# Optimization experiments

Measured on AMD Instinct MI355X. Metric: run time of the kernel, lower is better.

## Reference

```python
import jax, jax.numpy as jnp
import numpy as np

EPS = 1e-5

def setup_inputs() -> dict:
    key = jax.random.key(0)
    ks = jax.random.split(key, 12)
    b, C, Hx = 8, 1024, 28          # x: (b, C, Hx, Hx); y: (b, C//2, 2*Hx, 2*Hx)
    C2 = C // 2
    r = C2 // 7                      # fc bottleneck = 73
    f32 = jnp.float32
    inp = {
        'y': jax.random.normal(ks[0], (b, C2, 2*Hx, 2*Hx), f32),
        'x': jax.random.normal(ks[1], (b, C, Hx, Hx), f32),
        'fc1_w': jax.random.normal(ks[2], (r, C2), f32) * 0.02,
        'fc2_w': jax.random.normal(ks[3], (C2, r), f32) * 0.02,
        'conv_w': jax.random.normal(ks[4], (C2, C, 1, 1), f32) * 0.02,
        'conv_b': jnp.zeros((C2,), f32),
        'conv1_w': jax.random.normal(ks[5], (C2, C2 * 4, 1, 1), f32) * 0.02,
        'conv1_b': jnp.zeros((C2,), f32),
        'bn_gamma': jnp.ones((C2,), f32),
        'bn_beta': jnp.zeros((C2,), f32),
        'bn_mean': jnp.zeros((C2,), f32),
        'bn_var': jnp.ones((C2,), f32),
        'dw_w': jax.random.normal(ks[6], (C, 1, 3, 3), f32) * 0.1,  # depthwise, groups=C
        'dw_b': jnp.zeros((C,), f32),
    }
    return inp

def reference(y, x, fc1_w, fc2_w, conv_w, conv_b, conv1_w, conv1_b,
              bn_gamma, bn_beta, bn_mean, bn_var, dw_w, dw_b):
    def bn(t):  # BatchNorm2d in eval mode (running stats); same bn module reused twice
        return (t - bn_mean[:, None, None]) * jax.lax.rsqrt(bn_var[:, None, None] + EPS) \
               * bn_gamma[:, None, None] + bn_beta[:, None, None]
    # SE channel attention on y
    s = jnp.mean(y, axis=(2, 3))                              # (b, C2) GAP
    s = jax.nn.relu(s @ fc1_w.T) @ fc2_w.T                    # bias-free FCs
    y1 = y * jax.nn.sigmoid(s)[:, :, None, None]
    # depthwise 3x3 conv on x
    x1 = jax.lax.conv_general_dilated(
        x, dw_w, (1, 1), ((1, 1), (1, 1)),
        feature_group_count=x.shape[1],
        dimension_numbers=('NCHW', 'OIHW', 'NCHW')) + dw_b[None, :, None, None]
    # np.cov per (b, c) map: rows are variables, ddof=1 -> (Xc @ Xc^T)/(W-1)
    Wn = x1.shape[-1]
    xc = x1 - jnp.mean(x1, axis=-1, keepdims=True)
    x2 = jnp.einsum('bchw,bcgw->bchg', xc, xc) / (Wn - 1)     # (b, C, H, H)
    # 1x1 conv C->C2, bn, sigmoid
    x2 = jnp.einsum('bchw,oc->bohw', x2, conv_w[:, :, 0, 0]) + conv_b[None, :, None, None]
    x2 = jax.nn.sigmoid(bn(x2))
    # bilinear upsample x2 (half-pixel == torch align_corners=False)
    def up2(t):
        bb, cc, hh, ww = t.shape
        return jax.image.resize(t, (bb, cc, 2 * hh, 2 * ww), method='bilinear')
    x_up = up2(x)
    x2_up = up2(x2)
    cat = jnp.concatenate([y1, x2_up, x_up], axis=1)          # (b, 4*C2, 2H, 2W)
    out = jnp.einsum('bchw,oc->bohw', cat, conv1_w[:, :, 0, 0]) + conv1_b[None, :, None, None]
    return jax.nn.relu(bn(out))
```

## Files before the change

kernel.cpp:

```cpp
#include <hip/hip_runtime.h>
#include <math.h>

#define EPSV 1e-5f
#define B 8
#define C 1024
#define C2 512
#define RK 73
#define HW 784
#define QW 3136

typedef __attribute__((ext_vector_type(8))) short bf16x8;
typedef __attribute__((ext_vector_type(4))) float f32x4;

__device__ __forceinline__ unsigned short f2bf(float f) {
    unsigned u = __float_as_uint(f);
    return (unsigned short)((u + 0x7fffu + ((u >> 16) & 1u)) >> 16);
}
__device__ __forceinline__ float ld_f(const float* p) { return *p; }
__device__ __forceinline__ float ld_f(const unsigned short* p) {
    return __uint_as_float(((unsigned)*p) << 16);
}
__device__ __forceinline__ void ld4f(const float* p, float* d) {
    float4 v = *(const float4*)p;
    d[0] = v.x; d[1] = v.y; d[2] = v.z; d[3] = v.w;
}
__device__ __forceinline__ void ld4f(const unsigned short* p, float* d) {
    uint2 u = *(const uint2*)p;
    d[0] = __uint_as_float((u.x & 0xffffu) << 16);
    d[1] = __uint_as_float(u.x & 0xffff0000u);
    d[2] = __uint_as_float((u.y & 0xffffu) << 16);
    d[3] = __uint_as_float(u.y & 0xffff0000u);
}

__global__ void zero_s0(float* __restrict__ s0) {
    s0[blockIdx.x * 256 + threadIdx.x] = 0.f;
}

__global__ void se_fc_kernel(const float* __restrict__ s0,
                             const float* __restrict__ fc1_w,
                             const float* __restrict__ fc2_w,
                             float* __restrict__ att) {
    int b = blockIdx.x;
    __shared__ float sv[C2];
    __shared__ float hv[RK];
    for (int i = threadIdx.x; i < C2; i += 256) sv[i] = s0[b * C2 + i] * (1.0f / QW);
    __syncthreads();
    if (threadIdx.x < RK) {
        float acc = 0.f;
        const float4* wr4 = (const float4*)(fc1_w + threadIdx.x * C2);
        const float4* sv4 = (const float4*)sv;
#pragma unroll 16
        for (int k = 0; k < C2 / 4; ++k) {
            float4 w4 = wr4[k], s4 = sv4[k];
            acc += w4.x * s4.x + w4.y * s4.y + w4.z * s4.z + w4.w * s4.w;
        }
        hv[threadIdx.x] = fmaxf(acc, 0.f);
    }
    __syncthreads();
    for (int o = threadIdx.x; o < C2; o += 256) {
        float acc = 0.f;
        const float* wr = fc2_w + o * RK;
#pragma unroll
        for (int j = 0; j < RK; ++j) acc += wr[j] * hv[j];
        att[b * C2 + o] = 1.f / (1.f + expf(-acc));
    }
}

__global__ void dwcov_kernel(const float* __restrict__ x,
                             const float* __restrict__ dw_w,
                             const float* __restrict__ dw_b,
                             unsigned short* __restrict__ cov) {
    int bc = blockIdx.x;
    int c = bc & (C - 1);
    __shared__ float xs[HW];
    __shared__ __align__(16) float x1[HW];
    __shared__ float rm[28];
    const float* px = x + (size_t)bc * HW;
    for (int i = threadIdx.x; i < HW; i += 256) xs[i] = px[i];
    float wk[9];
#pragma unroll
    for (int j = 0; j < 9; ++j) wk[j] = dw_w[c * 9 + j];
    float bias = dw_b[c];
    __syncthreads();
    for (int p = threadIdx.x; p < HW; p += 256) {
        int h = p / 28, w = p - h * 28;
        float acc = bias;
#pragma unroll
        for (int dh = 0; dh < 3; ++dh) {
            int hh = h + dh - 1;
            if (hh < 0 || hh >= 28) continue;
#pragma unroll
            for (int dw = 0; dw < 3; ++dw) {
                int ww = w + dw - 1;
                if (ww < 0 || ww >= 28) continue;
                acc += xs[hh * 28 + ww] * wk[dh * 3 + dw];
            }
        }
        x1[p] = acc;
    }
    __syncthreads();
    if (threadIdx.x < 28) {
        float s = 0.f;
        for (int w = 0; w < 28; ++w) s += x1[threadIdx.x * 28 + w];
        rm[threadIdx.x] = s * (1.f / 28.f);
    }
    __syncthreads();
    unsigned short* pc = cov + (size_t)bc * HW;
    for (int idx = threadIdx.x; idx < 406; idx += 256) {
        int h = (int)((sqrtf((float)(8 * idx + 1)) - 1.f) * 0.5f);
        while ((h + 1) * (h + 2) / 2 <= idx) ++h;
        while (h * (h + 1) / 2 > idx) --h;
        int g = idx - h * (h + 1) / 2;
        float mh = rm[h], mg = rm[g];
        const float4* xh = (const float4*)&x1[h * 28];
        const float4* xg = (const float4*)&x1[g * 28];
        float acc = 0.f;
#pragma unroll
        for (int w4 = 0; w4 < 7; ++w4) {
            float4 a = xh[w4], bq = xg[w4];
            acc += (a.x - mh) * (bq.x - mg);
            acc += (a.y - mh) * (bq.y - mg);
            acc += (a.z - mh) * (bq.z - mg);
            acc += (a.w - mh) * (bq.w - mg);
        }
        unsigned short v = f2bf(acc * (1.f / 27.f));
        pc[h * 28 + g] = v;
        pc[g * 28 + h] = v;
    }
}

__global__ void pack_w(const float* __restrict__ conv_w, const float* __restrict__ conv_b,
                       const float* __restrict__ conv1_w, const float* __restrict__ conv1_b,
                       const float* __restrict__ bn_g, const float* __restrict__ bn_b,
                       const float* __restrict__ bn_m, const float* __restrict__ bn_v,
                       const float* __restrict__ att,
                       unsigned short* __restrict__ w0b, unsigned short* __restrict__ w1y,
                       unsigned short* __restrict__ w1pT,
                       float* __restrict__ sA, float* __restrict__ sB0, float* __restrict__ sB1) {
    int o = blockIdx.x, t = threadIdx.x;
    {
        int c4 = t * 4;
        float4 w4 = *(const float4*)&conv_w[(size_t)o * C + c4];
        unsigned short pk[4] = { f2bf(w4.x), f2bf(w4.y), f2bf(w4.z), f2bf(w4.w) };
        *(uint2*)&w0b[(size_t)o * C + c4] = *(uint2*)pk;
    }
#pragma unroll
    for (int i = 0; i < 2; ++i) {
        int e = t + i * 256;
        if (e < 384) {
            int c4 = e * 4;
            float4 w4 = *(const float4*)&conv1_w[(size_t)o * 2048 + 512 + c4];
            unsigned short pk[4] = { f2bf(w4.x), f2bf(w4.y), f2bf(w4.z), f2bf(w4.w) };
            *(uint2*)&w1pT[(size_t)o * 1536 + c4] = *(uint2*)pk;
        }
    }
#pragma unroll
    for (int i = 0; i < 4; ++i) {
        int e = t + i * 256;
        int bb = e >> 7, c4 = (e & 127) * 4;
        float4 w4 = *(const float4*)&conv1_w[(size_t)o * 2048 + c4];
        float4 a4 = *(const float4*)&att[bb * C2 + c4];
        unsigned short pk[4] = { f2bf(w4.x * a4.x), f2bf(w4.y * a4.y),
                                 f2bf(w4.z * a4.z), f2bf(w4.w * a4.w) };
        *(uint2*)&w1y[((size_t)bb * C2 + o) * C2 + c4] = *(uint2*)pk;
    }
    if (t == 0) {
        float sc = rsqrtf(bn_v[o] + EPSV) * bn_g[o];
        float bi = bn_b[o] - bn_m[o] * sc;
        sA[o] = sc;
        sB0[o] = conv_b[o] * sc + bi;
        sB1[o] = conv1_b[o] * sc + bi;
    }
}

template<typename ST, bool GAP>
__global__ __launch_bounds__(256)
void transpose_pass(const ST* __restrict__ src, unsigned short* __restrict__ dst,
                    float* __restrict__ s0,
                    int rows, int cols, int dpitch, int doff) {
    int b = blockIdx.z;
    int c0 = blockIdx.y * 64, p0 = blockIdx.x * 64;
    __shared__ float ts[64][65];
    int tid = threadIdx.x;
    int pl4 = (tid & 15) * 4, rr = tid >> 4;
    const ST* sb = src + ((size_t)b * rows + c0) * cols + p0;
    if (p0 + pl4 < cols) {
#pragma unroll
        for (int j = 0; j < 4; ++j) {
            int cl = rr + j * 16;
            float d[4];
            ld4f(&sb[(size_t)cl * cols + pl4], d);
            ts[cl][pl4 + 0] = d[0]; ts[cl][pl4 + 1] = d[1];
            ts[cl][pl4 + 2] = d[2]; ts[cl][pl4 + 3] = d[3];
        }
    }
    __syncthreads();
    int pl2b = tid >> 3, cl0 = (tid & 7) * 8;
#pragma unroll
    for (int j = 0; j < 2; ++j) {
        int pl2 = pl2b + j * 32;
        if (p0 + pl2 < cols) {
            unsigned short pk[8];
#pragma unroll
            for (int i = 0; i < 8; ++i) pk[i] = f2bf(ts[cl0 + i][pl2]);
            *(uint4*)&dst[((size_t)b * cols + p0 + pl2) * dpitch + doff + c0 + cl0] = *(uint4*)pk;
        }
    }
    if (GAP) {
        if (tid < 64) {
            float s = 0.f;
#pragma unroll
            for (int i = 0; i < 64; ++i) s += ts[tid][i];
            atomicAdd(&s0[b * rows + c0 + tid], s);
        }
    }
}

template<int MODE, int K>
__global__ __launch_bounds__(256)
void mfma_gemm(const unsigned short* __restrict__ wpk,
               const unsigned short* __restrict__ bsrc,
               const unsigned short* __restrict__ Pb,
               const float* __restrict__ sA, const float* __restrict__ sB,
               void* __restrict__ outv) {
    constexpr int NIT = K / 64;
    constexpr int NT  = (MODE == 2) ? 49 : 98;
    constexpr int QN = NT >> 3, REM = NT & 7;
    int bx = blockIdx.x;
    int r = bx & 7, ii = bx >> 3;
    int og = ii & 7, s = ii >> 3;
    int cnt = QN + (r < REM ? 1 : 0);
    if (s >= cnt) return;
    int t = (r < REM ? r * (QN + 1) : REM * (QN + 1) + (r - REM) * QN) + s;
    int o0 = og * 64;
    int n0 = t * 64;
    int b = blockIdx.z;
    union SM {
        struct { __align__(16) unsigned short Wt[2][4096]; __align__(16) unsigned short At[2][4096]; } s;
        float pt[(MODE == 2) ? 64 * 84 : 4];
    };
    __shared__ SM sm;
    int tid = threadIdx.x;
    int lane = tid & 63, wv = tid >> 6;
    int ln = lane & 15, quad = lane >> 4;
    int o_w = (wv >> 1) * 32, q_w = (wv & 1) * 32;
    int r_ = tid >> 2, cq = tid & 3;
    int stw0 = r_ * 64 + ((( cq << 1)      ^ (r_ & 7)) << 3);
    int stw1 = r_ * 64 + ((((cq << 1) | 1) ^ (r_ & 7)) << 3);
    int rq0 = (( quad      ^ (ln & 7)) << 3);
    int rq1 = (((4 | quad) ^ (ln & 7)) << 3);
    const unsigned short* wp = (MODE == 2) ? wpk + (size_t)b * C2 * C2 : wpk;
    const unsigned short* wg = wp + (size_t)(o0 + r_) * K + cq * 16;
    const unsigned short* bg = bsrc + ((size_t)((MODE == 2) ? b * QW : 0) + n0 + r_) * K + cq * 16;

    uint4 stA_a0, stA_a1, stA_b0, stA_b1;
    uint4 stB_a0, stB_a1, stB_b0, stB_b1;
    uint4 stC_a0, stC_a1, stC_b0, stC_b1;
    uint4 stD_a0, stD_a1, stD_b0, stD_b1;

#define LD_STAGE(P, CH) {                                                   \
        P##_a0 = *(const uint4*)(wg + (size_t)(CH) * 64);                   \
        P##_a1 = *(const uint4*)(wg + (size_t)(CH) * 64 + 8);               \
        P##_b0 = *(const uint4*)(bg + (size_t)(CH) * 64);                   \
        P##_b1 = *(const uint4*)(bg + (size_t)(CH) * 64 + 8); }

#define ST_STAGE(P, BUF) {                                                  \
        *(uint4*)&sm.s.Wt[BUF][stw0] = P##_a0;                              \
        *(uint4*)&sm.s.Wt[BUF][stw1] = P##_a1;                              \
        *(uint4*)&sm.s.At[BUF][stw0] = P##_b0;                              \
        *(uint4*)&sm.s.At[BUF][stw1] = P##_b1; }

#define GEMM_BODY(BUF, P, CHW, CHL) {                                               \
        bf16x8 a0 = *(const bf16x8*)&sm.s.Wt[BUF][(o_w + ln) * 64 + rq0];           \
        bf16x8 a1 = *(const bf16x8*)&sm.s.Wt[BUF][(o_w + 16 + ln) * 64 + rq0];      \
        bf16x8 b0 = *(const bf16x8*)&sm.s.At[BUF][(q_w + ln) * 64 + rq0];           \
        bf16x8 b1 = *(const bf16x8*)&sm.s.At[BUF][(q_w + 16 + ln) * 64 + rq0];      \
        bf16x8 a2 = *(const bf16x8*)&sm.s.Wt[BUF][(o_w + ln) * 64 + rq1];           \
        bf16x8 a3 = *(const bf16x8*)&sm.s.Wt[BUF][(o_w + 16 + ln) * 64 + rq1];      \
        bf16x8 b2 = *(const bf16x8*)&sm.s.At[BUF][(q_w + ln) * 64 + rq1];           \
        bf16x8 b3 = *(const bf16x8*)&sm.s.At[BUF][(q_w + 16 + ln) * 64 + rq1];      \
        acc[0][0] = __builtin_amdgcn_mfma_f32_16x16x32_bf16(a0, b0, acc[0][0], 0, 0, 0); \
        acc[0][1] = __builtin_amdgcn_mfma_f32_16x16x32_bf16(a0, b1, acc[0][1], 0, 0, 0); \
        acc[1][0] = __builtin_amdgcn_mfma_f32_16x16x32_bf16(a1, b0, acc[1][0], 0, 0, 0); \
        acc[1][1] = __builtin_amdgcn_mfma_f32_16x16x32_bf16(a1, b1, acc[1][1], 0, 0, 0); \
        acc[0][0] = __builtin_amdgcn_mfma_f32_16x16x32_bf16(a2, b2, acc[0][0], 0, 0, 0); \
        acc[0][1] = __builtin_amdgcn_mfma_f32_16x16x32_bf16(a2, b3, acc[0][1], 0, 0, 0); \
        acc[1][0] = __builtin_amdgcn_mfma_f32_16x16x32_bf16(a3, b2, acc[1][0], 0, 0, 0); \
        acc[1][1] = __builtin_amdgcn_mfma_f32_16x16x32_bf16(a3, b3, acc[1][1], 0, 0, 0); \
        if ((CHW) < NIT) {                                                          \
            ST_STAGE(P, (BUF) ^ 1)                                                  \
            if ((CHL) < NIT) LD_STAGE(P, (CHL))                                     \
            asm volatile("s_waitcnt lgkmcnt(0)" ::: "memory");                      \
            __builtin_amdgcn_s_barrier();                                           \
            __builtin_amdgcn_sched_barrier(0);                                      \
        } }

    LD_STAGE(stA, 0)
    ST_STAGE(stA, 0)
    LD_STAGE(stB, 1)
    LD_STAGE(stC, 2)
    LD_STAGE(stD, 3)
    LD_STAGE(stA, 4)
    asm volatile("s_waitcnt lgkmcnt(0)" ::: "memory");
    __builtin_amdgcn_s_barrier();
    __builtin_amdgcn_sched_barrier(0);

    f32x4 acc[2][2] = {};
    for (int i2 = 0; i2 < NIT; i2 += 4) {
        GEMM_BODY(0, stB, i2 + 1, i2 + 5)
        GEMM_BODY(1, stC, i2 + 2, i2 + 6)
        GEMM_BODY(0, stD, i2 + 3, i2 + 7)
        GEMM_BODY(1, stA, i2 + 4, i2 + 8)
    }
#undef GEMM_BODY
#undef ST_STAGE
#undef LD_STAGE

    if (MODE == 2) {
        float* outp = (float*)outv;
        int h0 = n0 / 56;
        int hmin = (h0 & 1) ? (h0 >> 1) : max(0, (h0 >> 1) - 1);
        float stv[21];
#pragma unroll
        for (int j = 0; j < 21; ++j) {
            int e = tid + j * 256;
            int o_l = e / 84, rem = e - o_l * 84;
            int s2 = rem / 28, w = rem - s2 * 28;
            int row = min(hmin + s2, 27);
            stv[j] = ld_f(&Pb[((size_t)b * C2 + o0 + o_l) * HW + row * 28 + w]);
        }
        __syncthreads();
#pragma unroll
        for (int j = 0; j < 21; ++j) sm.pt[tid + j * 256] = stv[j];
        __syncthreads();
#pragma unroll
        for (int nt = 0; nt < 2; ++nt) {
            int q = n0 + q_w + nt * 16 + ln;
            int hq = q / 56, wq = q - hq * 56;
            int hm = hq >> 1, wm = wq >> 1;
            int hn = (hq & 1) ? min(hm + 1, 27) : max(hm - 1, 0);
            int wn_ = (wq & 1) ? min(wm + 1, 27) : max(wm - 1, 0);
            int rm_ = (hm - hmin) * 28, rn_ = (hn - hmin) * 28;
#pragma unroll
            for (int mt = 0; mt < 2; ++mt)
#pragma unroll
                for (int reg = 0; reg < 4; ++reg) {
                    int ol = o_w + mt * 16 + quad * 4 + reg;
                    int o = o0 + ol;
                    const float* Pt = &sm.pt[ol * 84];
                    float up = 0.5625f * Pt[rm_ + wm] + 0.1875f * (Pt[rm_ + wn_] + Pt[rn_ + wm])
                             + 0.0625f * Pt[rn_ + wn_];
                    float v = (acc[mt][nt][reg] + up) * sA[o] + sB[o];
                    outp[((size_t)b * C2 + o) * QW + q] = fmaxf(v, 0.f);
                }
        }
    } else if (MODE == 0) {
        unsigned short* outp = (unsigned short*)outv;
#pragma unroll
        for (int nt = 0; nt < 2; ++nt) {
            int n = n0 + q_w + nt * 16 + ln;
#pragma unroll
            for (int mt = 0; mt < 2; ++mt) {
                int ob = o0 + o_w + mt * 16 + quad * 4;
                unsigned short pk[4];
#pragma unroll
                for (int reg = 0; reg < 4; ++reg) {
                    int o = ob + reg;
                    float v = acc[mt][nt][reg] * sA[o] + sB[o];
                    pk[reg] = f2bf(1.f / (1.f + expf(-v)));
                }
                *(uint2*)&outp[(size_t)n * 1536 + ob] = *(uint2*)pk;
            }
        }
    } else {
        unsigned short* outp = (unsigned short*)outv;
#pragma unroll
        for (int nt = 0; nt < 2; ++nt) {
            int n = n0 + q_w + nt * 16 + ln;
            int be = n / HW, pe = n - be * HW;
#pragma unroll
            for (int mt = 0; mt < 2; ++mt)
#pragma unroll
                for (int reg = 0; reg < 4; ++reg) {
                    int o = o0 + o_w + mt * 16 + quad * 4 + reg;
                    outp[((size_t)be * C2 + o) * HW + pe] = f2bf(acc[mt][nt][reg]);
                }
        }
    }
}

extern "C" void kernel_launch(void* const* d_in, const int* in_sizes, int n_in,
                              void* d_out, int out_size, void* d_ws, size_t ws_size,
                              hipStream_t stream) {
    const float* y       = (const float*)d_in[0];
    const float* x       = (const float*)d_in[1];
    const float* fc1_w   = (const float*)d_in[2];
    const float* fc2_w   = (const float*)d_in[3];
    const float* conv_w  = (const float*)d_in[4];
    const float* conv_b  = (const float*)d_in[5];
    const float* conv1_w = (const float*)d_in[6];
    const float* conv1_b = (const float*)d_in[7];
    const float* bn_g    = (const float*)d_in[8];
    const float* bn_b    = (const float*)d_in[9];
    const float* bn_m    = (const float*)d_in[10];
    const float* bn_v    = (const float*)d_in[11];
    const float* dw_w    = (const float*)d_in[12];
    const float* dw_b    = (const float*)d_in[13];
    float* out = (float*)d_out;

    unsigned short* cov_bf = (unsigned short*)d_out;
    unsigned short* covT   = cov_bf + (size_t)B * C * HW;
    unsigned short* BcatT  = covT + (size_t)B * HW * C;

    float* ws  = (float*)d_ws;
    float* s0  = ws;
    float* att = ws + 4096;
    float* sA  = ws + 8192;
    float* sB0 = ws + 8704;
    float* sB1 = ws + 9216;
    unsigned short* w0b  = (unsigned short*)(ws + 9728);
    unsigned short* w1y  = w0b + (size_t)C2 * C;
    unsigned short* w1pT = w1y + (size_t)B * C2 * C2;
    unsigned short* yT   = w1pT + (size_t)C2 * 1536;
    unsigned short* Pb   = yT + (size_t)B * QW * C2;

    zero_s0<<<16, 256, 0, stream>>>(s0);
    transpose_pass<float, true><<<dim3(49, 8, B), 256, 0, stream>>>(
        y, yT, s0, C2, QW, C2, 0);
    se_fc_kernel<<<B, 256, 0, stream>>>(s0, fc1_w, fc2_w, att);
    pack_w<<<C2, 256, 0, stream>>>(conv_w, conv_b, conv1_w, conv1_b,
                                   bn_g, bn_b, bn_m, bn_v, att,
                                   w0b, w1y, w1pT, sA, sB0, sB1);
    dwcov_kernel<<<B * C, 256, 0, stream>>>(x, dw_w, dw_b, cov_bf);
    transpose_pass<float, false><<<dim3(13, 16, B), 256, 0, stream>>>(
        x, BcatT, nullptr, C, HW, 1536, 512);
    transpose_pass<unsigned short, false><<<dim3(13, 16, B), 256, 0, stream>>>(
        cov_bf, covT, nullptr, C, HW, C, 0);
    mfma_gemm<0, 1024><<<dim3(832), 256, 0, stream>>>(w0b, covT, nullptr, sA, sB0, BcatT);
    mfma_gemm<1, 1536><<<dim3(832), 256, 0, stream>>>(w1pT, BcatT, nullptr, sA, sB0, Pb);
    mfma_gemm<2, 512><<<dim3(448, 1, B), 256, 0, stream>>>(w1y, yT, Pb, sA, sB1, out);
}
```

Before: 284.8 us.

## Fuse cov transpose into MODE-0 GEMM loads and process two channels per dwcov block

Removes the separate bf16 transpose of the covariance tensor. The MODE-0 GEMM now reads channel-major cov directly, using strided 32-bit loads that it repacks into the swizzled shared-memory layout, and tiles per batch over 13 pixel tiles. The depthwise/cov kernel handles two channels per block with float4 loads, which halves the block count. This saves a full read-write pass over the cov tensor and one launch, at the cost of less coalesced GEMM operand loads and some padded work on the last pixel tile.

Result: faster. 274.1 us (-3.8%).

```diff
diff --git a/kernel.cpp b/kernel.cpp
--- a/kernel.cpp
+++ b/kernel.cpp
@@ -71,61 +71,78 @@
                              const float* __restrict__ dw_b,
                              unsigned short* __restrict__ cov) {
     int bc = blockIdx.x;
-    int c = bc & (C - 1);
-    __shared__ float xs[HW];
-    __shared__ __align__(16) float x1[HW];
-    __shared__ float rm[28];
-    const float* px = x + (size_t)bc * HW;
-    for (int i = threadIdx.x; i < HW; i += 256) xs[i] = px[i];
-    float wk[9];
-#pragma unroll
-    for (int j = 0; j < 9; ++j) wk[j] = dw_w[c * 9 + j];
-    float bias = dw_b[c];
-    __syncthreads();
-    for (int p = threadIdx.x; p < HW; p += 256) {
-        int h = p / 28, w = p - h * 28;
-        float acc = bias;
-#pragma unroll
-        for (int dh = 0; dh < 3; ++dh) {
-            int hh = h + dh - 1;
-            if (hh < 0 || hh >= 28) continue;
-#pragma unroll
-            for (int dw = 0; dw < 3; ++dw) {
-                int ww = w + dw - 1;
-                if (ww < 0 || ww >= 28) continue;
-                acc += xs[hh * 28 + ww] * wk[dh * 3 + dw];
+    int b = bc >> 9, c0 = (bc & 511) << 1;
+    __shared__ __align__(16) float xs[2 * HW];
+    __shared__ __align__(16) float x1[2 * HW];
+    __shared__ float rm[2][28];
+    int tid = threadIdx.x;
+    const float* px = x + ((size_t)b * C + c0) * HW;
+#pragma unroll
+    for (int i4 = 0; i4 < 2; ++i4) {
+        int e = tid + i4 * 256;
+        if (e < 392) *(float4*)&xs[e * 4] = *(const float4*)&px[e * 4];
+    }
+    float wk0[9], wk1[9];
+#pragma unroll
+    for (int j = 0; j < 9; ++j) { wk0[j] = dw_w[c0 * 9 + j]; wk1[j] = dw_w[c0 * 9 + 9 + j]; }
+    float bi0 = dw_b[c0], bi1 = dw_b[c0 + 1];
+    __syncthreads();
+#pragma unroll
+    for (int ch = 0; ch < 2; ++ch) {
+        const float* xsc = &xs[ch * HW];
+        float* x1c = &x1[ch * HW];
+        float bias = ch ? bi1 : bi0;
+        for (int p = tid; p < HW; p += 256) {
+            int h = p / 28, w = p - h * 28;
+            float acc = bias;
+#pragma unroll
+            for (int dh = 0; dh < 3; ++dh) {
+                int hh = h + dh - 1;
+                if (hh < 0 || hh >= 28) continue;
+#pragma unroll
+                for (int dw = 0; dw < 3; ++dw) {
+                    int ww = w + dw - 1;
+                    if (ww < 0 || ww >= 28) continue;
+                    acc += xsc[hh * 28 + ww] * (ch ? wk1[dh * 3 + dw] : wk0[dh * 3 + dw]);
+                }
             }
-        }
-        x1[p] = acc;
-    }
-    __syncthreads();
-    if (threadIdx.x < 28) {
+            x1c[p] = acc;
+        }
+    }
+    __syncthreads();
+    if (tid < 56) {
+        int ch = tid >= 28 ? 1 : 0, hh = tid - 28 * ch;
+        const float* x1c = &x1[ch * HW];
         float s = 0.f;
-        for (int w = 0; w < 28; ++w) s += x1[threadIdx.x * 28 + w];
-        rm[threadIdx.x] = s * (1.f / 28.f);
-    }
-    __syncthreads();
-    unsigned short* pc = cov + (size_t)bc * HW;
-    for (int idx = threadIdx.x; idx < 406; idx += 256) {
-        int h = (int)((sqrtf((float)(8 * idx + 1)) - 1.f) * 0.5f);
-        while ((h + 1) * (h + 2) / 2 <= idx) ++h;
-        while (h * (h + 1) / 2 > idx) --h;
-        int g = idx - h * (h + 1) / 2;
-        float mh = rm[h], mg = rm[g];
-        const float4* xh = (const float4*)&x1[h * 28];
-        const float4* xg = (const float4*)&x1[g * 28];
-        float acc = 0.f;
-#pragma unroll
-        for (int w4 = 0; w4 < 7; ++w4) {
-            float4 a = xh[w4], bq = xg[w4];
-            acc += (a.x - mh) * (bq.x - mg);
-            acc += (a.y - mh) * (bq.y - mg);
-            acc += (a.z - mh) * (bq.z - mg);
-            acc += (a.w - mh) * (bq.w - mg);
-        }
-        unsigned short v = f2bf(acc * (1.f / 27.f));
-        pc[h * 28 + g] = v;
-        pc[g * 28 + h] = v;
+        for (int w = 0; w < 28; ++w) s += x1c[hh * 28 + w];
+        rm[ch][hh] = s * (1.f / 28.f);
+    }
+    __syncthreads();
+#pragma unroll
+    for (int ch = 0; ch < 2; ++ch) {
+        unsigned short* pc = cov + ((size_t)b * C + c0 + ch) * HW;
+        const float* x1c = &x1[ch * HW];
+        for (int idx = tid; idx < 406; idx += 256) {
+            int h = (int)((sqrtf((float)(8 * idx + 1)) - 1.f) * 0.5f);
+            while ((h + 1) * (h + 2) / 2 <= idx) ++h;
+            while (h * (h + 1) / 2 > idx) --h;
+            int g = idx - h * (h + 1) / 2;
+            float mh = rm[ch][h], mg = rm[ch][g];
+            const float4* xh = (const float4*)&x1c[h * 28];
+            const float4* xg = (const float4*)&x1c[g * 28];
+            float acc = 0.f;
+#pragma unroll
+            for (int w4 = 0; w4 < 7; ++w4) {
+                float4 a = xh[w4], bq = xg[w4];
+                acc += (a.x - mh) * (bq.x - mg);
+                acc += (a.y - mh) * (bq.y - mg);
+                acc += (a.z - mh) * (bq.z - mg);
+                acc += (a.w - mh) * (bq.w - mg);
+            }
+            unsigned short v = f2bf(acc * (1.f / 27.f));
+            pc[h * 28 + g] = v;
+            pc[g * 28 + h] = v;
+        }
     }
 }
 
@@ -224,7 +241,7 @@
                const float* __restrict__ sA, const float* __restrict__ sB,
                void* __restrict__ outv) {
     constexpr int NIT = K / 64;
-    constexpr int NT  = (MODE == 2) ? 49 : 98;
+    constexpr int NT  = (MODE == 1) ? 98 : ((MODE == 0) ? 13 : 49);
     constexpr int QN = NT >> 3, REM = NT & 7;
     int bx = blockIdx.x;
     int r = bx & 7, ii = bx >> 3;
@@ -251,24 +268,57 @@
     int rq1 = (((4 | quad) ^ (ln & 7)) << 3);
     const unsigned short* wp = (MODE == 2) ? wpk + (size_t)b * C2 * C2 : wpk;
     const unsigned short* wg = wp + (size_t)(o0 + r_) * K + cq * 16;
-    const unsigned short* bg = bsrc + ((size_t)((MODE == 2) ? b * QW : 0) + n0 + r_) * K + cq * 16;
+    const unsigned short* bg = nullptr;
+    const unsigned short* bgs = nullptr;
+    int n0l = 0, kg = 0, bw0 = 0, bw1 = 0;
+    if (MODE == 0) {
+        n0l = (tid & 31) * 2;
+        kg = tid >> 5;
+        int pg = min(n0 + n0l, HW - 2);
+        bgs = bsrc + ((size_t)b * C + kg * 8) * HW + pg;
+        bw0 = n0l * 64 + ((kg ^ (n0l & 7)) << 3);
+        bw1 = (n0l + 1) * 64 + ((kg ^ ((n0l + 1) & 7)) << 3);
+    } else {
+        bg = bsrc + ((size_t)((MODE == 2) ? b * QW : 0) + n0 + r_) * K + cq * 16;
+    }
 
     uint4 stA_a0, stA_a1, stA_b0, stA_b1;
     uint4 stB_a0, stB_a1, stB_b0, stB_b1;
     uint4 stC_a0, stC_a1, stC_b0, stC_b1;
     uint4 stD_a0, stD_a1, stD_b0, stD_b1;
+    unsigned stA_u[8], stB_u[8], stC_u[8], stD_u[8];
 
 #define LD_STAGE(P, CH) {                                                   \
         P##_a0 = *(const uint4*)(wg + (size_t)(CH) * 64);                   \
         P##_a1 = *(const uint4*)(wg + (size_t)(CH) * 64 + 8);               \
-        P##_b0 = *(const uint4*)(bg + (size_t)(CH) * 64);                   \
-        P##_b1 = *(const uint4*)(bg + (size_t)(CH) * 64 + 8); }
+        if (MODE == 0) {                                                    \
+            _Pragma("unroll")                                               \
+            for (int _j = 0; _j < 8; ++_j)                                  \
+                P##_u[_j] = *(const unsigned*)(bgs + (size_t)((CH) * 64 + _j) * HW); \
+        } else {                                                            \
+            P##_b0 = *(const uint4*)(bg + (size_t)(CH) * 64);               \
+            P##_b1 = *(const uint4*)(bg + (size_t)(CH) * 64 + 8);           \
+        } }
 
 #define ST_STAGE(P, BUF) {                                                  \
         *(uint4*)&sm.s.Wt[BUF][stw0] = P##_a0;                              \
         *(uint4*)&sm.s.Wt[BUF][stw1] = P##_a1;                              \
-        *(uint4*)&sm.s.At[BUF][stw0] = P##_b0;                              \
-        *(uint4*)&sm.s.At[BUF][stw1] = P##_b1; }
+        if (MODE == 0) {                                                    \
+            uint4 _lo, _hi;                                                 \
+            _lo.x = (P##_u[0] & 0xffffu) | (P##_u[1] << 16);                \
+            _lo.y = (P##_u[2] & 0xffffu) | (P##_u[3] << 16);                \
+            _lo.z = (P##_u[4] & 0xffffu) | (P##_u[5] << 16);                \
+            _lo.w = (P##_u[6] & 0xffffu) | (P##_u[7] << 16);                \
+            _hi.x = (P##_u[0] >> 16) | (P##_u[1] & 0xffff0000u);            \
+            _hi.y = (P##_u[2] >> 16) | (P##_u[3] & 0xffff0000u);            \
+            _hi.z = (P##_u[4] >> 16) | (P##_u[5] & 0xffff0000u);            \
+            _hi.w = (P##_u[6] >> 16) | (P##_u[7] & 0xffff0000u);            \
+            *(uint4*)&sm.s.At[BUF][bw0] = _lo;                              \
+            *(uint4*)&sm.s.At[BUF][bw1] = _hi;                              \
+        } else {                                                            \
+            *(uint4*)&sm.s.At[BUF][stw0] = P##_b0;                          \
+            *(uint4*)&sm.s.At[BUF][stw1] = P##_b1;                          \
+        } }
 
 #define GEMM_BODY(BUF, P, CHW, CHL) {                                               \
         bf16x8 a0 = *(const bf16x8*)&sm.s.Wt[BUF][(o_w + ln) * 64 + rq0];           \
@@ -358,18 +408,21 @@
         unsigned short* outp = (unsigned short*)outv;
 #pragma unroll
         for (int nt = 0; nt < 2; ++nt) {
-            int n = n0 + q_w + nt * 16 + ln;
-#pragma unroll
-            for (int mt = 0; mt < 2; ++mt) {
-                int ob = o0 + o_w + mt * 16 + quad * 4;
-                unsigned short pk[4];
-#pragma unroll
-                for (int reg = 0; reg < 4; ++reg) {
-                    int o = ob + reg;
-                    float v = acc[mt][nt][reg] * sA[o] + sB[o];
-                    pk[reg] = f2bf(1.f / (1.f + expf(-v)));
+            int p = n0 + q_w + nt * 16 + ln;
+            if (p < HW) {
+                size_t n = (size_t)b * HW + p;
+#pragma unroll
+                for (int mt = 0; mt < 2; ++mt) {
+                    int ob = o0 + o_w + mt * 16 + quad * 4;
+                    unsigned short pk[4];
+#pragma unroll
+                    for (int reg = 0; reg < 4; ++reg) {
+                        int o = ob + reg;
+                        float v = acc[mt][nt][reg] * sA[o] + sB[o];
+                        pk[reg] = f2bf(1.f / (1.f + expf(-v)));
+                    }
+                    *(uint2*)&outp[n * 1536 + ob] = *(uint2*)pk;
                 }
-                *(uint2*)&outp[(size_t)n * 1536 + ob] = *(uint2*)pk;
             }
         }
     } else {
@@ -409,8 +462,7 @@
     float* out = (float*)d_out;
 
     unsigned short* cov_bf = (unsigned short*)d_out;
-    unsigned short* covT   = cov_bf + (size_t)B * C * HW;
-    unsigned short* BcatT  = covT + (size_t)B * HW * C;
+    unsigned short* BcatT  = cov_bf + (size_t)B * C * HW;
 
     float* ws  = (float*)d_ws;
     float* s0  = ws;
@@ -431,12 +483,10 @@
     pack_w<<<C2, 256, 0, stream>>>(conv_w, conv_b, conv1_w, conv1_b,
                                    bn_g, bn_b, bn_m, bn_v, att,
                                    w0b, w1y, w1pT, sA, sB0, sB1);
-    dwcov_kernel<<<B * C, 256, 0, stream>>>(x, dw_w, dw_b, cov_bf);
+    dwcov_kernel<<<B * C / 2, 256, 0, stream>>>(x, dw_w, dw_b, cov_bf);
     transpose_pass<float, false><<<dim3(13, 16, B), 256, 0, stream>>>(
         x, BcatT, nullptr, C, HW, 1536, 512);
-    transpose_pass<unsigned short, false><<<dim3(13, 16, B), 256, 0, stream>>>(
-        cov_bf, covT, nullptr, C, HW, C, 0);
-    mfma_gemm<0, 1024><<<dim3(832), 256, 0, stream>>>(w0b, covT, nullptr, sA, sB0, BcatT);
+    mfma_gemm<0, 1024><<<dim3(128, 1, B), 256, 0, stream>>>(w0b, cov_bf, nullptr, sA, sB0, BcatT);
     mfma_gemm<1, 1536><<<dim3(832), 256, 0, stream>>>(w1pT, BcatT, nullptr, sA, sB0, Pb);
     mfma_gemm<2, 512><<<dim3(448, 1, B), 256, 0, stream>>>(w1y, yT, Pb, sA, sB1, out);
 }
```
